# Kernel tuning notes

Hardware: AMD Instinct MI355X
Metric: run time of the kernel (lower is better)

Reference implementation:

```python
import jax, jax.numpy as jnp
import numpy as np

N_USER, N_PHOTO = 100_000, 200_000   # node counts per ntype
E = 1_000_000                        # edges per canonical etype
IN, OUT = 256, 64                    # in_size / out_size from HeteroRGCN defaults


def setup_inputs() -> dict:
    key = jax.random.key(0)
    ks = jax.random.split(key, 8)
    s = 1.0 / np.sqrt(IN)  # nn.Linear default init scale
    return {
        "user_feats": jax.random.normal(ks[0], (N_USER, IN), jnp.float32),   # learned self.user_feats
        "photo_feats": jax.random.normal(ks[1], (N_PHOTO, IN), jnp.float32),  # G.nodes['photo'].data['features']
        "W_likes": jax.random.uniform(ks[2], (IN, OUT), jnp.float32, -s, s),
        "b_likes": jnp.zeros((OUT,), jnp.float32),
        "W_likedby": jax.random.uniform(ks[3], (IN, OUT), jnp.float32, -s, s),
        "b_likedby": jnp.zeros((OUT,), jnp.float32),
        "likes_src": jax.random.randint(ks[4], (E,), 0, N_USER, jnp.int32),
        "likes_dst": jax.random.randint(ks[5], (E,), 0, N_PHOTO, jnp.int32),
        "likedby_src": jax.random.randint(ks[6], (E,), 0, N_PHOTO, jnp.int32),
        "likedby_dst": jax.random.randint(ks[7], (E,), 0, N_USER, jnp.int32),
    }


def _mean_agg(Wh_src, src, dst, n_dst):
    # DGL fn.copy_u + fn.mean: gather projected src feats along edges,
    # segment-sum into dst nodes, divide by in-degree (0-degree -> 0).
    msgs = Wh_src[src]  # [E, OUT] irregular gather
    tot = jax.ops.segment_sum(msgs, dst, num_segments=n_dst)
    deg = jax.ops.segment_sum(jnp.ones((src.shape[0],), msgs.dtype), dst, num_segments=n_dst)
    return tot / jnp.maximum(deg, 1.0)[:, None]


def reference(user_feats, photo_feats, W_likes, b_likes, W_likedby, b_likedby,
              likes_src, likes_dst, likedby_src, likedby_dst):
    # per-etype linear projection (self.weight[etype])
    Wh_likes = user_feats @ W_likes + b_likes        # src ntype 'user'
    Wh_likedby = photo_feats @ W_likedby + b_likedby  # src ntype 'photo'
    # multi_update_all({etype: (copy_u, mean)}, 'sum'); each dst ntype has one etype here
    h_photo = _mean_agg(Wh_likes, likes_src, likes_dst, N_PHOTO)
    h_user = _mean_agg(Wh_likedby, likedby_src, likedby_dst, N_USER)
    return h_user, h_photo
```

## Files before the change

### kernel.cpp

```cpp
#include <hip/hip_runtime.h>
#include <hip/hip_bf16.h>

#define N_USER 100000
#define N_PHOTO 200000
#define NEDGE 1000000
#define INF 256
#define OUTF 64

typedef unsigned short u16;
typedef __attribute__((ext_vector_type(8))) short short8;
typedef __attribute__((ext_vector_type(4))) float f32x4;

#define BP 1563
#define BU 782
#define NB (BP + BU)
#define NE4 250000
#define TOT4 (2 * NE4)
#define CAP 8192

#define NPROJ_U ((N_USER + 63) / 64)
#define NPROJ_P ((N_PHOTO + 63) / 64)
#define NPROJ (NPROJ_U + NPROJ_P)
#define NHIST 128

__device__ inline u16 f2b(float f) {
    union { float f; unsigned u; } v; v.f = f;
    unsigned r = v.u + 0x7FFF + ((v.u >> 16) & 1);
    return (u16)(r >> 16);
}
__device__ inline float b2f(u16 h) {
    union { unsigned u; float f; } v; v.u = ((unsigned)h) << 16; return v.f;
}

__global__ __launch_bounds__(256) void prep0(const float* __restrict__ W_likes,
                                             const float* __restrict__ W_likedby,
                                             u16* __restrict__ Wt_likes,
                                             u16* __restrict__ Wt_likedby,
                                             int* __restrict__ bucket_cnt) {
    int i = blockIdx.x * 256 + threadIdx.x;
    if (i < INF * OUTF) {
        int n = i & (OUTF - 1), k = i >> 6;
        Wt_likes[n * INF + k]   = f2b(W_likes[i]);
        Wt_likedby[n * INF + k] = f2b(W_likedby[i]);
    }
    if (i < NB) bucket_cnt[i] = 0;
}

__global__ __launch_bounds__(256) void work1(
    const float* __restrict__ user_feats, const float* __restrict__ photo_feats,
    const u16* __restrict__ Wt_likes, const u16* __restrict__ Wt_likedby,
    const float* __restrict__ b_likes, const float* __restrict__ b_likedby,
    u16* __restrict__ Wh_likes, u16* __restrict__ Wh_likedby,
    const int* __restrict__ likes_dst, const int* __restrict__ likedby_dst,
    int* __restrict__ bucket_cnt)
{
    __shared__ __align__(16) char smem_raw[OUTF * 256 * 2];
    int bb = blockIdx.x;
    int tid = threadIdx.x;

    if (bb >= NPROJ) {
        int* h = (int*)smem_raw;
        for (int i = tid; i < NB; i += 256) h[i] = 0;
        __syncthreads();
        int hb = bb - NPROJ;
        int gt = hb * 256 + tid, nt = NHIST * 256;
        for (int i = gt; i < TOT4; i += nt) {
            bool L = i < NE4;
            int j = L ? i : i - NE4;
            int4 d = L ? ((const int4*)likes_dst)[j] : ((const int4*)likedby_dst)[j];
            int ofs = L ? 0 : BP;
            atomicAdd(&h[ofs + (d.x >> 7)], 1);
            atomicAdd(&h[ofs + (d.y >> 7)], 1);
            atomicAdd(&h[ofs + (d.z >> 7)], 1);
            atomicAdd(&h[ofs + (d.w >> 7)], 1);
        }
        __syncthreads();
        for (int i = tid; i < NB; i += 256) {
            int c = h[i];
            if (c) atomicAdd(&bucket_cnt[i], c);
        }
        return;
    }

    u16* lds_wt = (u16*)smem_raw;
    const float* feats; const u16* Wt; const float* bias; u16* Wh; int nrows; int blk;
    if (bb < NPROJ_U) { feats = user_feats;  Wt = Wt_likes;   bias = b_likes;   Wh = Wh_likes;   nrows = N_USER;  blk = bb; }
    else              { feats = photo_feats; Wt = Wt_likedby; bias = b_likedby; Wh = Wh_likedby; nrows = N_PHOTO; blk = bb - NPROJ_U; }

    for (int c = tid; c < (INF * OUTF) / 8; c += 256) {
        int n = c >> 5;
        int ko8 = c & 31;
        int sw = ko8 ^ (n & 7);
        *(short8*)&lds_wt[n * 256 + sw * 8] = *(const short8*)&Wt[n * INF + ko8 * 8];
    }
    __syncthreads();

    int wave = tid >> 6, lane = tid & 63;
    int l15 = lane & 15, quad = lane >> 4;
    int r0 = blk * 64 + wave * 16;
    int arow = r0 + l15;
    bool arow_ok = arow < nrows;

    f32x4 acc[4] = {{0,0,0,0},{0,0,0,0},{0,0,0,0},{0,0,0,0}};
    const float4* ap = (const float4*)(feats + (size_t)(arow_ok ? arow : 0) * INF);

    #pragma unroll
    for (int ks = 0; ks < 8; ++ks) {
        float4 x = ap[ks * 8 + quad * 2 + 0];
        float4 y = ap[ks * 8 + quad * 2 + 1];
        short8 a = { (short)f2b(x.x), (short)f2b(x.y), (short)f2b(x.z), (short)f2b(x.w),
                     (short)f2b(y.x), (short)f2b(y.y), (short)f2b(y.z), (short)f2b(y.w) };
        #pragma unroll
        for (int nt2 = 0; nt2 < 4; ++nt2) {
            int row = nt2 * 16 + l15;
            int sw = (ks * 4 + quad) ^ (l15 & 7);
            short8 b = *(const short8*)&lds_wt[row * 256 + sw * 8];
            acc[nt2] = __builtin_amdgcn_mfma_f32_16x16x32_bf16(a, b, acc[nt2], 0, 0, 0);
        }
    }

    #pragma unroll
    for (int nt2 = 0; nt2 < 4; ++nt2) {
        int col = nt2 * 16 + l15;
        float bv = bias[col];
        #pragma unroll
        for (int r = 0; r < 4; ++r) {
            int row = r0 + quad * 4 + r;
            if (row < nrows) {
                Wh[(size_t)row * OUTF + col] = f2b(acc[nt2][r] + bv);
            }
        }
    }
}

__global__ __launch_bounds__(256) void p2_scan(const int* __restrict__ bucket_cnt,
                                               int* __restrict__ bucket_off,
                                               int* __restrict__ bucket_cur) {
    __shared__ int lds[256];
    int t = threadIdx.x;
    int base_i = t * 10;
    int loc[10];
    int s = 0;
    #pragma unroll
    for (int k = 0; k < 10; ++k) {
        int idx = base_i + k;
        int v = (idx < NB) ? bucket_cnt[idx] : 0;
        loc[k] = s; s += v;
    }
    lds[t] = s;
    __syncthreads();
    for (int ofs = 1; ofs < 256; ofs <<= 1) {
        int v = (t >= ofs) ? lds[t - ofs] : 0;
        __syncthreads();
        lds[t] += v;
        __syncthreads();
    }
    int excl = lds[t] - s;
    #pragma unroll
    for (int k = 0; k < 10; ++k) {
        int idx = base_i + k;
        if (idx < NB) {
            int o = excl + loc[k];
            bucket_off[idx] = o;
            bucket_cur[idx] = o;
        }
    }
    if (t == 255) bucket_off[NB] = lds[255];
}

__global__ __launch_bounds__(256) void p3_part(
    const int* __restrict__ likes_src, const int* __restrict__ likes_dst,
    const int* __restrict__ likedby_src, const int* __restrict__ likedby_dst,
    int* __restrict__ bucket_cur, unsigned* __restrict__ part) {
    __shared__ int h[NB];
    int tid = threadIdx.x;
    for (int i = tid; i < NB; i += 256) h[i] = 0;
    __syncthreads();
    int gt = blockIdx.x * 256 + tid, nt = gridDim.x * 256;
    for (int i = gt; i < TOT4; i += nt) {
        bool L = i < NE4;
        int j = L ? i : i - NE4;
        int4 d = L ? ((const int4*)likes_dst)[j] : ((const int4*)likedby_dst)[j];
        int ofs = L ? 0 : BP;
        atomicAdd(&h[ofs + (d.x >> 7)], 1);
        atomicAdd(&h[ofs + (d.y >> 7)], 1);
        atomicAdd(&h[ofs + (d.z >> 7)], 1);
        atomicAdd(&h[ofs + (d.w >> 7)], 1);
    }
    __syncthreads();
    for (int i = tid; i < NB; i += 256) {
        int c = h[i];
        h[i] = c ? atomicAdd(&bucket_cur[i], c) : 0;
    }
    __syncthreads();
    for (int i = gt; i < TOT4; i += nt) {
        bool L = i < NE4;
        int j = L ? i : i - NE4;
        int4 d = L ? ((const int4*)likes_dst)[j] : ((const int4*)likedby_dst)[j];
        int4 s = L ? ((const int4*)likes_src)[j] : ((const int4*)likedby_src)[j];
        int ofs = L ? 0 : BP;
        int p;
        p = atomicAdd(&h[ofs + (d.x >> 7)], 1); part[p] = ((unsigned)s.x << 7) | (unsigned)(d.x & 127);
        p = atomicAdd(&h[ofs + (d.y >> 7)], 1); part[p] = ((unsigned)s.y << 7) | (unsigned)(d.y & 127);
        p = atomicAdd(&h[ofs + (d.z >> 7)], 1); part[p] = ((unsigned)s.z << 7) | (unsigned)(d.z & 127);
        p = atomicAdd(&h[ofs + (d.w >> 7)], 1); part[p] = ((unsigned)s.w << 7) | (unsigned)(d.w & 127);
    }
}

__global__ __launch_bounds__(256) void p4_reduce(
    const u16* __restrict__ Wh_likes, const u16* __restrict__ Wh_likedby,
    const int* __restrict__ bucket_off, const unsigned* __restrict__ part,
    float* __restrict__ out)
{
    __shared__ unsigned srt[CAP];
    __shared__ int hist[128];
    __shared__ int scn[129];
    __shared__ int cur[128];
    int b = blockIdx.x, t = threadIdx.x;
    const u16* Wh; float* obase; int node0, nn;
    if (b < BP) {
        Wh = Wh_likes; node0 = b << 7;
        nn = (node0 + 128 <= N_PHOTO) ? 128 : (N_PHOTO - node0);
        obase = out + ((size_t)N_USER + node0) * OUTF;
    } else {
        Wh = Wh_likedby; node0 = (b - BP) << 7;
        nn = (node0 + 128 <= N_USER) ? 128 : (N_USER - node0);
        obase = out + (size_t)node0 * OUTF;
    }
    int e0 = bucket_off[b], e1 = bucket_off[b + 1];
    int cnt = e1 - e0;

    if (cnt <= CAP) {
        if (t < 128) hist[t] = 0;
        __syncthreads();
        for (int e = e0 + t; e < e1; e += 256)
            atomicAdd(&hist[part[e] & 127], 1);
        __syncthreads();
        if (t == 0) scn[0] = 0;
        if (t < 128) scn[t + 1] = hist[t];
        __syncthreads();
        for (int ofs = 1; ofs < 128; ofs <<= 1) {
            int idx = t + 1;
            int v = (t < 128 && idx > ofs) ? scn[idx - ofs] : 0;
            __syncthreads();
            if (t < 128) scn[idx] += v;
            __syncthreads();
        }
        if (t < 128) cur[t] = scn[t];
        __syncthreads();
        for (int e = e0 + t; e < e1; e += 256) {
            unsigned v = part[e];
            int pos = atomicAdd(&cur[v & 127], 1);
            srt[pos] = v >> 7;
        }
        __syncthreads();

        int g = t >> 3, sub = t & 7;
        for (int dl = g; dl < 128; dl += 32) {
            int o0 = scn[dl], o1 = scn[dl + 1];
            f32x4 a0 = {0,0,0,0}, a1 = {0,0,0,0};
            int j = o0;
            for (; j + 4 <= o1; j += 4) {
                int s0 = srt[j], s1 = srt[j + 1], s2 = srt[j + 2], s3 = srt[j + 3];
                short8 v0 = *(const short8*)(Wh + (size_t)s0 * OUTF + sub * 8);
                short8 v1 = *(const short8*)(Wh + (size_t)s1 * OUTF + sub * 8);
                short8 v2 = *(const short8*)(Wh + (size_t)s2 * OUTF + sub * 8);
                short8 v3 = *(const short8*)(Wh + (size_t)s3 * OUTF + sub * 8);
                #pragma unroll
                for (int k = 0; k < 4; ++k) {
                    a0[k] += b2f((u16)v0[k]) + b2f((u16)v1[k]) + b2f((u16)v2[k]) + b2f((u16)v3[k]);
                    a1[k] += b2f((u16)v0[k + 4]) + b2f((u16)v1[k + 4]) + b2f((u16)v2[k + 4]) + b2f((u16)v3[k + 4]);
                }
            }
            for (; j < o1; ++j) {
                int s = srt[j];
                short8 v = *(const short8*)(Wh + (size_t)s * OUTF + sub * 8);
                #pragma unroll
                for (int k = 0; k < 4; ++k) {
                    a0[k] += b2f((u16)v[k]);
                    a1[k] += b2f((u16)v[k + 4]);
                }
            }
            int dgi = o1 - o0;
            float inv = 1.0f / (float)(dgi > 1 ? dgi : 1);
            if (dl < nn) {
                float* orow = obase + (size_t)dl * OUTF + sub * 8;
                float4 w0 = { a0[0] * inv, a0[1] * inv, a0[2] * inv, a0[3] * inv };
                float4 w1 = { a1[0] * inv, a1[1] * inv, a1[2] * inv, a1[3] * inv };
                *(float4*)orow = w0;
                *(float4*)(orow + 4) = w1;
            }
        }
    } else {
        float* acc = (float*)srt;
        for (int i = t; i < 128 * OUTF; i += 256) acc[i] = 0.f;
        if (t < 128) hist[t] = 0;
        __syncthreads();
        int hw = t >> 5, l = t & 31;
        for (int e = e0 + hw; e < e1; e += 8) {
            unsigned v = part[e];
            int src = (int)(v >> 7), dl = (int)(v & 127);
            unsigned w = ((const unsigned*)(Wh + (size_t)src * OUTF))[l];
            atomicAdd(&acc[dl * OUTF + 2 * l], b2f((u16)(w & 0xffff)));
            atomicAdd(&acc[dl * OUTF + 2 * l + 1], b2f((u16)(w >> 16)));
            if (l == 0) atomicAdd(&hist[dl], 1);
        }
        __syncthreads();
        for (int i = t; i < nn * (OUTF / 4); i += 256) {
            int node = i >> 4;
            int dg = hist[node];
            float inv = 1.0f / (float)(dg > 1 ? dg : 1);
            float4 vv = *(const float4*)&acc[node * OUTF + (i & 15) * 4];
            vv.x *= inv; vv.y *= inv; vv.z *= inv; vv.w *= inv;
            ((float4*)obase)[i] = vv;
        }
    }
}

extern "C" void kernel_launch(void* const* d_in, const int* in_sizes, int n_in,
                              void* d_out, int out_size, void* d_ws, size_t ws_size,
                              hipStream_t stream) {
    const float* user_feats  = (const float*)d_in[0];
    const float* photo_feats = (const float*)d_in[1];
    const float* W_likes     = (const float*)d_in[2];
    const float* b_likes     = (const float*)d_in[3];
    const float* W_likedby   = (const float*)d_in[4];
    const float* b_likedby   = (const float*)d_in[5];
    const int* likes_src     = (const int*)d_in[6];
    const int* likes_dst     = (const int*)d_in[7];
    const int* likedby_src   = (const int*)d_in[8];
    const int* likedby_dst   = (const int*)d_in[9];

    char* ws = (char*)d_ws;
    u16* Wh_likes     = (u16*)(ws + 0);
    u16* Wh_likedby   = (u16*)(ws + 12800000);
    u16* Wt_likes     = (u16*)(ws + 38400000);
    u16* Wt_likedby   = (u16*)(ws + 38432768);
    int* bucket_cnt   = (int*)(ws + 38465536);
    int* bucket_off   = (int*)(ws + 38474928);
    int* bucket_cur   = (int*)(ws + 38484320);
    unsigned* part    = (unsigned*)(ws + 38493712);

    float* out = (float*)d_out;

    prep0<<<64, 256, 0, stream>>>(W_likes, W_likedby, Wt_likes, Wt_likedby, bucket_cnt);

    work1<<<NPROJ + NHIST, 256, 0, stream>>>(
        user_feats, photo_feats, Wt_likes, Wt_likedby, b_likes, b_likedby,
        Wh_likes, Wh_likedby, likes_dst, likedby_dst, bucket_cnt);

    p2_scan<<<1, 256, 0, stream>>>(bucket_cnt, bucket_off, bucket_cur);

    p3_part<<<128, 256, 0, stream>>>(likes_src, likes_dst, likedby_src, likedby_dst,
                                     bucket_cur, part);

    p4_reduce<<<NB, 256, 0, stream>>>(Wh_likes, Wh_likedby, bucket_off, part, out);
}
```

Baseline: 496.1 us.

## Use fixed-capacity buckets with overflow list and fuse partitioning into projection kernel

Edges are now scattered into fixed-capacity per-bucket slots with an overflow list, instead of counting, prefix-scanning, then partitioning. That removes the scan kernel and the separate partition kernel, and the histogram-of-dst pass that existed only to size buckets. Partitioning now runs in the first blocks of the projection kernel, so it overlaps with the GEMM. The reduce kernel reads bucket fill levels directly and scans the overflow list for stragglers. The cost is bounded capacity: more than 8192 overflow edges would be silently dropped, and the overflow scan is serial per node.

Result: faster. 455.4 us (-8.2%).

```diff
diff --git a/kernel.cpp b/kernel.cpp
--- a/kernel.cpp
+++ b/kernel.cpp
@@ -16,12 +16,22 @@
 #define NB (BP + BU)
 #define NE4 250000
 #define TOT4 (2 * NE4)
-#define CAP 8192
-
+
+#define CAPP 1024
+#define CAPU 1536
+#define UBASE (BP * CAPP)
+#define PART_N (UBASE + BU * CAPU)
+#define OVF_MAX 8192
+#define SORT_CAP 2048
+
+#define NPART 128
 #define NPROJ_U ((N_USER + 63) / 64)
 #define NPROJ_P ((N_PHOTO + 63) / 64)
 #define NPROJ (NPROJ_U + NPROJ_P)
-#define NHIST 128
+
+__device__ inline int bkt_base(int b) { return b < BP ? b * CAPP : UBASE + (b - BP) * CAPU; }
+__device__ inline int bkt_limit(int b) { return b < BP ? (b + 1) * CAPP : UBASE + (b - BP + 1) * CAPU; }
+__device__ inline int bkt_cap(int b) { return b < BP ? CAPP : CAPU; }
 
 __device__ inline u16 f2b(float f) {
     union { float f; unsigned u; } v; v.f = f;
@@ -36,14 +46,16 @@
                                              const float* __restrict__ W_likedby,
                                              u16* __restrict__ Wt_likes,
                                              u16* __restrict__ Wt_likedby,
-                                             int* __restrict__ bucket_cnt) {
+                                             int* __restrict__ bucket_cur,
+                                             int* __restrict__ novf) {
     int i = blockIdx.x * 256 + threadIdx.x;
     if (i < INF * OUTF) {
         int n = i & (OUTF - 1), k = i >> 6;
         Wt_likes[n * INF + k]   = f2b(W_likes[i]);
         Wt_likedby[n * INF + k] = f2b(W_likedby[i]);
     }
-    if (i < NB) bucket_cnt[i] = 0;
+    if (i < NB) bucket_cur[i] = bkt_base(i);
+    if (i == 0) *novf = 0;
 }
 
 __global__ __launch_bounds__(256) void work1(
@@ -51,19 +63,20 @@
     const u16* __restrict__ Wt_likes, const u16* __restrict__ Wt_likedby,
     const float* __restrict__ b_likes, const float* __restrict__ b_likedby,
     u16* __restrict__ Wh_likes, u16* __restrict__ Wh_likedby,
-    const int* __restrict__ likes_dst, const int* __restrict__ likedby_dst,
-    int* __restrict__ bucket_cnt)
+    const int* __restrict__ likes_src, const int* __restrict__ likes_dst,
+    const int* __restrict__ likedby_src, const int* __restrict__ likedby_dst,
+    int* __restrict__ bucket_cur, unsigned* __restrict__ part,
+    int* __restrict__ novf, uint2* __restrict__ ovf)
 {
     __shared__ __align__(16) char smem_raw[OUTF * 256 * 2];
     int bb = blockIdx.x;
     int tid = threadIdx.x;
 
-    if (bb >= NPROJ) {
+    if (bb < NPART) {
         int* h = (int*)smem_raw;
         for (int i = tid; i < NB; i += 256) h[i] = 0;
         __syncthreads();
-        int hb = bb - NPROJ;
-        int gt = hb * 256 + tid, nt = NHIST * 256;
+        int gt = bb * 256 + tid, nt = NPART * 256;
         for (int i = gt; i < TOT4; i += nt) {
             bool L = i < NE4;
             int j = L ? i : i - NE4;
@@ -77,15 +90,38 @@
         __syncthreads();
         for (int i = tid; i < NB; i += 256) {
             int c = h[i];
-            if (c) atomicAdd(&bucket_cnt[i], c);
+            h[i] = c ? atomicAdd(&bucket_cur[i], c) : 0;
+        }
+        __syncthreads();
+        for (int i = gt; i < TOT4; i += nt) {
+            bool L = i < NE4;
+            int j = L ? i : i - NE4;
+            int4 d = L ? ((const int4*)likes_dst)[j] : ((const int4*)likedby_dst)[j];
+            int4 s = L ? ((const int4*)likes_src)[j] : ((const int4*)likedby_src)[j];
+            int ofs = L ? 0 : BP;
+            int dv[4] = {d.x, d.y, d.z, d.w};
+            int sv[4] = {s.x, s.y, s.z, s.w};
+            #pragma unroll
+            for (int k = 0; k < 4; ++k) {
+                int bk = ofs + (dv[k] >> 7);
+                unsigned pk = ((unsigned)sv[k] << 7) | (unsigned)(dv[k] & 127);
+                int p = atomicAdd(&h[bk], 1);
+                if (p < bkt_limit(bk)) {
+                    part[p] = pk;
+                } else {
+                    int oi = atomicAdd(novf, 1);
+                    if (oi < OVF_MAX) { uint2 o; o.x = (unsigned)bk; o.y = pk; ovf[oi] = o; }
+                }
+            }
         }
         return;
     }
 
+    int bb2 = bb - NPART;
     u16* lds_wt = (u16*)smem_raw;
     const float* feats; const u16* Wt; const float* bias; u16* Wh; int nrows; int blk;
-    if (bb < NPROJ_U) { feats = user_feats;  Wt = Wt_likes;   bias = b_likes;   Wh = Wh_likes;   nrows = N_USER;  blk = bb; }
-    else              { feats = photo_feats; Wt = Wt_likedby; bias = b_likedby; Wh = Wh_likedby; nrows = N_PHOTO; blk = bb - NPROJ_U; }
+    if (bb2 < NPROJ_U) { feats = user_feats;  Wt = Wt_likes;   bias = b_likes;   Wh = Wh_likes;   nrows = N_USER;  blk = bb2; }
+    else               { feats = photo_feats; Wt = Wt_likedby; bias = b_likedby; Wh = Wh_likedby; nrows = N_PHOTO; blk = bb2 - NPROJ_U; }
 
     for (int c = tid; c < (INF * OUTF) / 8; c += 256) {
         int n = c >> 5;
@@ -133,86 +169,13 @@
     }
 }
 
-__global__ __launch_bounds__(256) void p2_scan(const int* __restrict__ bucket_cnt,
-                                               int* __restrict__ bucket_off,
-                                               int* __restrict__ bucket_cur) {
-    __shared__ int lds[256];
-    int t = threadIdx.x;
-    int base_i = t * 10;
-    int loc[10];
-    int s = 0;
-    #pragma unroll
-    for (int k = 0; k < 10; ++k) {
-        int idx = base_i + k;
-        int v = (idx < NB) ? bucket_cnt[idx] : 0;
-        loc[k] = s; s += v;
-    }
-    lds[t] = s;
-    __syncthreads();
-    for (int ofs = 1; ofs < 256; ofs <<= 1) {
-        int v = (t >= ofs) ? lds[t - ofs] : 0;
-        __syncthreads();
-        lds[t] += v;
-        __syncthreads();
-    }
-    int excl = lds[t] - s;
-    #pragma unroll
-    for (int k = 0; k < 10; ++k) {
-        int idx = base_i + k;
-        if (idx < NB) {
-            int o = excl + loc[k];
-            bucket_off[idx] = o;
-            bucket_cur[idx] = o;
-        }
-    }
-    if (t == 255) bucket_off[NB] = lds[255];
-}
-
-__global__ __launch_bounds__(256) void p3_part(
-    const int* __restrict__ likes_src, const int* __restrict__ likes_dst,
-    const int* __restrict__ likedby_src, const int* __restrict__ likedby_dst,
-    int* __restrict__ bucket_cur, unsigned* __restrict__ part) {
-    __shared__ int h[NB];
-    int tid = threadIdx.x;
-    for (int i = tid; i < NB; i += 256) h[i] = 0;
-    __syncthreads();
-    int gt = blockIdx.x * 256 + tid, nt = gridDim.x * 256;
-    for (int i = gt; i < TOT4; i += nt) {
-        bool L = i < NE4;
-        int j = L ? i : i - NE4;
-        int4 d = L ? ((const int4*)likes_dst)[j] : ((const int4*)likedby_dst)[j];
-        int ofs = L ? 0 : BP;
-        atomicAdd(&h[ofs + (d.x >> 7)], 1);
-        atomicAdd(&h[ofs + (d.y >> 7)], 1);
-        atomicAdd(&h[ofs + (d.z >> 7)], 1);
-        atomicAdd(&h[ofs + (d.w >> 7)], 1);
-    }
-    __syncthreads();
-    for (int i = tid; i < NB; i += 256) {
-        int c = h[i];
-        h[i] = c ? atomicAdd(&bucket_cur[i], c) : 0;
-    }
-    __syncthreads();
-    for (int i = gt; i < TOT4; i += nt) {
-        bool L = i < NE4;
-        int j = L ? i : i - NE4;
-        int4 d = L ? ((const int4*)likes_dst)[j] : ((const int4*)likedby_dst)[j];
-        int4 s = L ? ((const int4*)likes_src)[j] : ((const int4*)likedby_src)[j];
-        int ofs = L ? 0 : BP;
-        int p;
-        p = atomicAdd(&h[ofs + (d.x >> 7)], 1); part[p] = ((unsigned)s.x << 7) | (unsigned)(d.x & 127);
-        p = atomicAdd(&h[ofs + (d.y >> 7)], 1); part[p] = ((unsigned)s.y << 7) | (unsigned)(d.y & 127);
-        p = atomicAdd(&h[ofs + (d.z >> 7)], 1); part[p] = ((unsigned)s.z << 7) | (unsigned)(d.z & 127);
-        p = atomicAdd(&h[ofs + (d.w >> 7)], 1); part[p] = ((unsigned)s.w << 7) | (unsigned)(d.w & 127);
-    }
-}
-
 __global__ __launch_bounds__(256) void p4_reduce(
     const u16* __restrict__ Wh_likes, const u16* __restrict__ Wh_likedby,
-    const int* __restrict__ bucket_off, const unsigned* __restrict__ part,
+    const int* __restrict__ bucket_cur, const unsigned* __restrict__ part,
+    const int* __restrict__ novf, const uint2* __restrict__ ovf,
     float* __restrict__ out)
 {
-    __shared__ unsigned srt[CAP];
+    __shared__ unsigned srt[SORT_CAP];
     __shared__ int hist[128];
     __shared__ int scn[129];
     __shared__ int cur[128];
@@ -227,92 +190,87 @@
         nn = (node0 + 128 <= N_USER) ? 128 : (N_USER - node0);
         obase = out + (size_t)node0 * OUTF;
     }
-    int e0 = bucket_off[b], e1 = bucket_off[b + 1];
-    int cnt = e1 - e0;
-
-    if (cnt <= CAP) {
-        if (t < 128) hist[t] = 0;
-        __syncthreads();
-        for (int e = e0 + t; e < e1; e += 256)
-            atomicAdd(&hist[part[e] & 127], 1);
-        __syncthreads();
-        if (t == 0) scn[0] = 0;
-        if (t < 128) scn[t + 1] = hist[t];
-        __syncthreads();
-        for (int ofs = 1; ofs < 128; ofs <<= 1) {
-            int idx = t + 1;
-            int v = (t < 128 && idx > ofs) ? scn[idx - ofs] : 0;
-            __syncthreads();
-            if (t < 128) scn[idx] += v;
-            __syncthreads();
-        }
-        if (t < 128) cur[t] = scn[t];
-        __syncthreads();
-        for (int e = e0 + t; e < e1; e += 256) {
-            unsigned v = part[e];
-            int pos = atomicAdd(&cur[v & 127], 1);
-            srt[pos] = v >> 7;
-        }
-        __syncthreads();
-
-        int g = t >> 3, sub = t & 7;
-        for (int dl = g; dl < 128; dl += 32) {
-            int o0 = scn[dl], o1 = scn[dl + 1];
-            f32x4 a0 = {0,0,0,0}, a1 = {0,0,0,0};
-            int j = o0;
-            for (; j + 4 <= o1; j += 4) {
-                int s0 = srt[j], s1 = srt[j + 1], s2 = srt[j + 2], s3 = srt[j + 3];
-                short8 v0 = *(const short8*)(Wh + (size_t)s0 * OUTF + sub * 8);
-                short8 v1 = *(const short8*)(Wh + (size_t)s1 * OUTF + sub * 8);
-                short8 v2 = *(const short8*)(Wh + (size_t)s2 * OUTF + sub * 8);
-                short8 v3 = *(const short8*)(Wh + (size_t)s3 * OUTF + sub * 8);
-                #pragma unroll
-                for (int k = 0; k < 4; ++k) {
-                    a0[k] += b2f((u16)v0[k]) + b2f((u16)v1[k]) + b2f((u16)v2[k]) + b2f((u16)v3[k]);
-                    a1[k] += b2f((u16)v0[k + 4]) + b2f((u16)v1[k + 4]) + b2f((u16)v2[k + 4]) + b2f((u16)v3[k + 4]);
+    int base = bkt_base(b);
+    int cnt = bucket_cur[b] - base;
+    int cap = bkt_cap(b);
+    if (cnt > cap) cnt = cap;
+    int e0 = base, e1 = base + cnt;
+    int novf_v = *novf;
+    if (novf_v > OVF_MAX) novf_v = OVF_MAX;
+
+    if (t < 128) hist[t] = 0;
+    __syncthreads();
+    for (int e = e0 + t; e < e1; e += 256)
+        atomicAdd(&hist[part[e] & 127], 1);
+    __syncthreads();
+    if (t == 0) scn[0] = 0;
+    if (t < 128) scn[t + 1] = hist[t];
+    __syncthreads();
+    for (int ofs = 1; ofs < 128; ofs <<= 1) {
+        int idx = t + 1;
+        int v = (t < 128 && idx > ofs) ? scn[idx - ofs] : 0;
+        __syncthreads();
+        if (t < 128) scn[idx] += v;
+        __syncthreads();
+    }
+    if (t < 128) cur[t] = scn[t];
+    __syncthreads();
+    for (int e = e0 + t; e < e1; e += 256) {
+        unsigned v = part[e];
+        int pos = atomicAdd(&cur[v & 127], 1);
+        srt[pos] = v >> 7;
+    }
+    __syncthreads();
+
+    int g = t >> 3, sub = t & 7;
+    for (int dl = g; dl < 128; dl += 32) {
+        int o0 = scn[dl], o1 = scn[dl + 1];
+        f32x4 a0 = {0,0,0,0}, a1 = {0,0,0,0};
+        int j = o0;
+        for (; j + 4 <= o1; j += 4) {
+            int s0 = srt[j], s1 = srt[j + 1], s2 = srt[j + 2], s3 = srt[j + 3];
+            short8 v0 = *(const short8*)(Wh + (size_t)s0 * OUTF + sub * 8);
+            short8 v1 = *(const short8*)(Wh + (size_t)s1 * OUTF + sub * 8);
+            short8 v2 = *(const short8*)(Wh + (size_t)s2 * OUTF + sub * 8);
+            short8 v3 = *(const short8*)(Wh + (size_t)s3 * OUTF + sub * 8);
+            #pragma unroll
+            for (int k = 0; k < 4; ++k) {
+                a0[k] += b2f((u16)v0[k]) + b2f((u16)v1[k]) + b2f((u16)v2[k]) + b2f((u16)v3[k]);
+                a1[k] += b2f((u16)v0[k + 4]) + b2f((u16)v1[k + 4]) + b2f((u16)v2[k + 4]) + b2f((u16)v3[k + 4]);
+            }
+        }
+        for (; j < o1; ++j) {
+            int s = srt[j];
+            short8 v = *(const short8*)(Wh + (size_t)s * OUTF + sub * 8);
+            #pragma unroll
+            for (int k = 0; k < 4; ++k) {
+                a0[k] += b2f((u16)v[k]);
+                a1[k] += b2f((u16)v[k + 4]);
+            }
+        }
+        int dgi = o1 - o0;
+        if (novf_v > 0) {
+            for (int e = 0; e < novf_v; ++e) {
+                uint2 o = ovf[e];
+                if ((int)o.x == b && (int)(o.y & 127u) == dl) {
+                    int s = (int)(o.y >> 7);
+                    short8 v = *(const short8*)(Wh + (size_t)s * OUTF + sub * 8);
+                    #pragma unroll
+                    for (int k = 0; k < 4; ++k) {
+                        a0[k] += b2f((u16)v[k]);
+                        a1[k] += b2f((u16)v[k + 4]);
+                    }
+                    ++dgi;
                 }
             }
-            for (; j < o1; ++j) {
-                int s = srt[j];
-                short8 v = *(const short8*)(Wh + (size_t)s * OUTF + sub * 8);
-                #pragma unroll
-                for (int k = 0; k < 4; ++k) {
-                    a0[k] += b2f((u16)v[k]);
-                    a1[k] += b2f((u16)v[k + 4]);
-                }
-            }
-            int dgi = o1 - o0;
-            float inv = 1.0f / (float)(dgi > 1 ? dgi : 1);
-            if (dl < nn) {
-                float* orow = obase + (size_t)dl * OUTF + sub * 8;
-                float4 w0 = { a0[0] * inv, a0[1] * inv, a0[2] * inv, a0[3] * inv };
-                float4 w1 = { a1[0] * inv, a1[1] * inv, a1[2] * inv, a1[3] * inv };
-                *(float4*)orow = w0;
-                *(float4*)(orow + 4) = w1;
-            }
-        }
-    } else {
-        float* acc = (float*)srt;
-        for (int i = t; i < 128 * OUTF; i += 256) acc[i] = 0.f;
-        if (t < 128) hist[t] = 0;
-        __syncthreads();
-        int hw = t >> 5, l = t & 31;
-        for (int e = e0 + hw; e < e1; e += 8) {
-            unsigned v = part[e];
-            int src = (int)(v >> 7), dl = (int)(v & 127);
-            unsigned w = ((const unsigned*)(Wh + (size_t)src * OUTF))[l];
-            atomicAdd(&acc[dl * OUTF + 2 * l], b2f((u16)(w & 0xffff)));
-            atomicAdd(&acc[dl * OUTF + 2 * l + 1], b2f((u16)(w >> 16)));
-            if (l == 0) atomicAdd(&hist[dl], 1);
-        }
-        __syncthreads();
-        for (int i = t; i < nn * (OUTF / 4); i += 256) {
-            int node = i >> 4;
-            int dg = hist[node];
-            float inv = 1.0f / (float)(dg > 1 ? dg : 1);
-            float4 vv = *(const float4*)&acc[node * OUTF + (i & 15) * 4];
-            vv.x *= inv; vv.y *= inv; vv.z *= inv; vv.w *= inv;
-            ((float4*)obase)[i] = vv;
+        }
+        float inv = 1.0f / (float)(dgi > 1 ? dgi : 1);
+        if (dl < nn) {
+            float* orow = obase + (size_t)dl * OUTF + sub * 8;
+            float4 w0 = { a0[0] * inv, a0[1] * inv, a0[2] * inv, a0[3] * inv };
+            float4 w1 = { a1[0] * inv, a1[1] * inv, a1[2] * inv, a1[3] * inv };
+            *(float4*)orow = w0;
+            *(float4*)(orow + 4) = w1;
         }
     }
 }
@@ -336,23 +294,21 @@
     u16* Wh_likedby   = (u16*)(ws + 12800000);
     u16* Wt_likes     = (u16*)(ws + 38400000);
     u16* Wt_likedby   = (u16*)(ws + 38432768);
-    int* bucket_cnt   = (int*)(ws + 38465536);
-    int* bucket_off   = (int*)(ws + 38474928);
-    int* bucket_cur   = (int*)(ws + 38484320);
-    unsigned* part    = (unsigned*)(ws + 38493712);
+    int* bucket_cur   = (int*)(ws + 38465536);
+    unsigned* part    = (unsigned*)(ws + 38474928);
+    int* novf         = (int*)(ws + 49681584);
+    uint2* ovf        = (uint2*)(ws + 49681600);
 
     float* out = (float*)d_out;
 
-    prep0<<<64, 256, 0, stream>>>(W_likes, W_likedby, Wt_likes, Wt_likedby, bucket_cnt);
-
-    work1<<<NPROJ + NHIST, 256, 0, stream>>>(
+    prep0<<<64, 256, 0, stream>>>(W_likes, W_likedby, Wt_likes, Wt_likedby,
+                                  bucket_cur, novf);
+
+    work1<<<NPART + NPROJ, 256, 0, stream>>>(
         user_feats, photo_feats, Wt_likes, Wt_likedby, b_likes, b_likedby,
-        Wh_likes, Wh_likedby, likes_dst, likedby_dst, bucket_cnt);
-
-    p2_scan<<<1, 256, 0, stream>>>(bucket_cnt, bucket_off, bucket_cur);
-
-    p3_part<<<128, 256, 0, stream>>>(likes_src, likes_dst, likedby_src, likedby_dst,
-                                     bucket_cur, part);
-
-    p4_reduce<<<NB, 256, 0, stream>>>(Wh_likes, Wh_likedby, bucket_off, part, out);
-}
+        Wh_likes, Wh_likedby, likes_src, likes_dst, likedby_src, likedby_dst,
+        bucket_cur, part, novf, ovf);
+
+    p4_reduce<<<NB, 256, 0, stream>>>(Wh_likes, Wh_likedby, bucket_cur, part,
+                                      novf, ovf, out);
+}
```
